# Kernel optimization log

Measured on AMD Instinct MI355X. Metric: run time of the kernel, lower is better.

The kernel has to match this reference:

```python
import jax, jax.numpy as jnp
import numpy as np

NEG_SLOPE = 0.2


def gat_conv(x, src, dst, W, a_src, a_dst, bias, concat, num_nodes):
    # x: [N, F_in]; W: [F_in, H*C]; a_src/a_dst: [H, C]
    H, C = a_src.shape
    h = (x @ W).reshape(num_nodes, H, C)               # [N,H,C]
    alpha_s = jnp.sum(h * a_src[None], axis=-1)        # [N,H]
    alpha_d = jnp.sum(h * a_dst[None], axis=-1)        # [N,H]
    e = jax.nn.leaky_relu(alpha_s[src] + alpha_d[dst], NEG_SLOPE)  # [E,H]
    m = jax.ops.segment_max(e, dst, num_segments=num_nodes)
    m = jnp.where(jnp.isfinite(m), m, 0.0)
    ex = jnp.exp(e - m[dst])
    denom = jax.ops.segment_sum(ex, dst, num_segments=num_nodes)
    alpha = ex / (denom[dst] + 1e-16)                  # scatter-softmax over dst
    msg = h[src] * alpha[:, :, None]                   # [E,H,C]
    out = jax.ops.segment_sum(msg, dst, num_segments=num_nodes)  # [N,H,C]
    if concat:
        out = out.reshape(num_nodes, H * C)
    else:
        out = out.mean(axis=1)
    return out + bias


def setup_inputs() -> dict:
    key = jax.random.key(0)
    ks = jax.random.split(key, 12)
    N, E = 50000, 800000
    num_concat, F_in, hid, H1, H2, n_cls = 2, 128, 64, 4, 1, 16
    x_list = jax.random.normal(ks[0], (num_concat, N, F_in), dtype=jnp.float32)
    edge_index = jax.random.randint(ks[1], (2, E), 0, N, dtype=jnp.int64)
    s = 0.1
    W1 = jax.random.normal(ks[2], (num_concat, F_in, H1 * hid), dtype=jnp.float32) * s
    att_src1 = jax.random.normal(ks[3], (num_concat, H1, hid), dtype=jnp.float32) * s
    att_dst1 = jax.random.normal(ks[4], (num_concat, H1, hid), dtype=jnp.float32) * s
    bias1 = jnp.zeros((num_concat, H1 * hid), dtype=jnp.float32)
    W2 = jax.random.normal(ks[5], (hid * H1 * num_concat, H2 * n_cls), dtype=jnp.float32) * s
    att_src2 = jax.random.normal(ks[6], (H2, n_cls), dtype=jnp.float32) * s
    att_dst2 = jax.random.normal(ks[7], (H2, n_cls), dtype=jnp.float32) * s
    bias2 = jnp.zeros((n_cls,), dtype=jnp.float32)
    return {"x_list": x_list, "edge_index": edge_index,
            "W1": W1, "att_src1": att_src1, "att_dst1": att_dst1, "bias1": bias1,
            "W2": W2, "att_src2": att_src2, "att_dst2": att_dst2, "bias2": bias2}


def reference(x_list, edge_index, W1, att_src1, att_dst1, bias1, W2, att_src2, att_dst2, bias2):
    num_concat, N, _ = x_list.shape
    loop = jnp.arange(N, dtype=edge_index.dtype)
    src = jnp.concatenate([edge_index[0], loop])  # PyG add_self_loops=True
    dst = jnp.concatenate([edge_index[1], loop])
    hidden = [jax.nn.elu(gat_conv(x_list[k], src, dst, W1[k], att_src1[k], att_dst1[k],
                                  bias1[k], True, N))
              for k in range(num_concat)]
    x = jnp.concatenate(hidden, axis=-1)           # [N, hid*H1*num_concat]
    out = gat_conv(x, src, dst, W2, att_src2, att_dst2, bias2, False, N)
    return out
```

## Files before the change

### kernel.cpp

```cpp
#include <hip/hip_runtime.h>

#define LEAKY(v) ((v) >= 0.0f ? (v) : 0.2f * (v))

typedef __attribute__((ext_vector_type(8))) short bf16x8;
typedef __attribute__((ext_vector_type(4))) float f32x4;

__device__ __forceinline__ unsigned short f2bf(float f) {
    unsigned int u = __float_as_uint(f);
    unsigned int r = u + 0x7FFFu + ((u >> 16) & 1u);
    return (unsigned short)(r >> 16);
}
__device__ __forceinline__ unsigned int pk2(float a, float b) {
    return (unsigned int)f2bf(a) | ((unsigned int)f2bf(b) << 16);
}
__device__ __forceinline__ float lo16(unsigned int u) { return __uint_as_float(u << 16); }
__device__ __forceinline__ float hi16(unsigned int u) { return __uint_as_float(u & 0xFFFF0000u); }


__global__ __launch_bounds__(256) void count_deg(const int* ei, int* deg, int E, int Etot) {
    int i = blockIdx.x * 256 + threadIdx.x;
    if (i >= Etot) return;
    int d = (i < E) ? ei[E + i] : (i - E);
    atomicAdd(&deg[d], 1);
}

__global__ __launch_bounds__(512) void scan_block(const int* deg, int* excl, int* bsum, int n) {
    __shared__ int s[512];
    int t = threadIdx.x;
    int i = blockIdx.x * 512 + t;
    int v = (i < n) ? deg[i] : 0;
    s[t] = v;
    __syncthreads();
    for (int d = 1; d < 512; d <<= 1) {
        int x = 0;
        if (t >= d) x = s[t - d];
        __syncthreads();
        if (t >= d) s[t] += x;
        __syncthreads();
    }
    if (i < n) excl[i] = s[t] - v;
    if (t == 511) bsum[blockIdx.x] = s[511];
}

__global__ __launch_bounds__(512) void scan_sums(const int* bsum, int* boff, int nb) {
    __shared__ int s[512];
    int t = threadIdx.x;
    int v = (t < nb) ? bsum[t] : 0;
    s[t] = v;
    __syncthreads();
    for (int d = 1; d < 512; d <<= 1) {
        int x = 0;
        if (t >= d) x = s[t - d];
        __syncthreads();
        if (t >= d) s[t] += x;
        __syncthreads();
    }
    boff[t] = s[t] - v;
}

__global__ __launch_bounds__(256) void finalize_off(int* csr, int* cursor, const int* boff, int n, int etot) {
    int i = blockIdx.x * 256 + threadIdx.x;
    if (i < n) {
        int v = csr[i] + boff[i >> 9];
        csr[i] = v;
        cursor[i] = v;
    }
    if (i == 0) csr[n] = etot;
}

__global__ __launch_bounds__(256) void scatter_src(const int* ei, int* cursor, int* srcs, int E, int Etot) {
    int i = blockIdx.x * 256 + threadIdx.x;
    if (i >= Etot) return;
    int s, d;
    if (i < E) { s = ei[i]; d = ei[E + i]; }
    else       { s = i - E; d = s; }
    int pos = atomicAdd(&cursor[d], 1);
    srcs[pos] = s;
}


__global__ __launch_bounds__(256) void wpack1(const float* __restrict__ W1, unsigned short* __restrict__ wt1) {
    int id = blockIdx.x * 256 + threadIdx.x;
    if (id >= 8192) return;
    int conv = id >> 12, rem = id & 4095;
    int c = rem >> 4, q = rem & 15;
    const float* src = W1 + (size_t)conv * 32768 + (size_t)(q * 8) * 256 + c;
    float w[8];
#pragma unroll
    for (int j = 0; j < 8; ++j) w[j] = src[j * 256];
    uint4 v;
    v.x = pk2(w[0], w[1]); v.y = pk2(w[2], w[3]);
    v.z = pk2(w[4], w[5]); v.w = pk2(w[6], w[7]);
    *(uint4*)(wt1 + (size_t)conv * 32768 + c * 128 + ((q ^ (c & 7)) << 3)) = v;
}

__global__ __launch_bounds__(256) void wpack2(const float* __restrict__ W2, unsigned short* __restrict__ wt2) {
    int id = blockIdx.x * 256 + threadIdx.x;
    if (id >= 1024) return;
    int s = id >> 6, l = id & 63;
    const float* src = W2 + (size_t)(s * 32 + (l >> 4) * 8) * 16 + (l & 15);
    float w[8];
#pragma unroll
    for (int j = 0; j < 8; ++j) w[j] = src[j * 16];
    uint4 v;
    v.x = pk2(w[0], w[1]); v.y = pk2(w[2], w[3]);
    v.z = pk2(w[4], w[5]); v.w = pk2(w[6], w[7]);
    *(uint4*)(wt2 + (size_t)id * 8) = v;
}


__global__ __launch_bounds__(256) void gemm1_mfma(const float* __restrict__ x_list,
                                                  const unsigned short* __restrict__ wt1,
                                                  const float* __restrict__ asw, const float* __restrict__ adw,
                                                  unsigned short* __restrict__ hp,
                                                  float* __restrict__ aad, int N) {
    __shared__ unsigned short As[64 * 128];
    __shared__ unsigned short Ws[256 * 128];
    int conv = blockIdx.y;
    int t = threadIdx.x;
    int w = t >> 6, l = t & 63;

    const float* xg = x_list + (size_t)conv * N * 128;
#pragma unroll
    for (int p = 0; p < 4; ++p) {
        int id = p * 256 + t;
        int row = id >> 4, q = id & 15;
        int grow = blockIdx.x * 64 + row;
        uint4 v = make_uint4(0, 0, 0, 0);
        if (grow < N) {
            const float* src = xg + (size_t)grow * 128 + q * 8;
            float4 a = *(const float4*)src;
            float4 b = *(const float4*)(src + 4);
            v.x = pk2(a.x, a.y); v.y = pk2(a.z, a.w);
            v.z = pk2(b.x, b.y); v.w = pk2(b.z, b.w);
        }
        *(uint4*)(As + row * 128 + ((q ^ (row & 7)) << 3)) = v;
    }
    const uint4* wsrc = (const uint4*)(wt1 + (size_t)conv * 32768);
#pragma unroll
    for (int p = 0; p < 16; ++p) {
        int id = p * 256 + t;
        *(uint4*)(Ws + (size_t)id * 8) = wsrc[id];
    }
    __syncthreads();

    f32x4 acc[4][4];
#pragma unroll
    for (int mt = 0; mt < 4; ++mt)
#pragma unroll
        for (int nt = 0; nt < 4; ++nt) acc[mt][nt] = (f32x4){0.f, 0.f, 0.f, 0.f};

    int lr = l & 15, lg = l >> 4;
#pragma unroll
    for (int s = 0; s < 4; ++s) {
        int kq = s * 4 + lg;
        bf16x8 af[4], bf[4];
#pragma unroll
        for (int mt = 0; mt < 4; ++mt) {
            int r = mt * 16 + lr;
            af[mt] = *(const bf16x8*)(As + r * 128 + ((kq ^ (r & 7)) << 3));
        }
#pragma unroll
        for (int nt = 0; nt < 4; ++nt) {
            int c = w * 64 + nt * 16 + lr;
            bf[nt] = *(const bf16x8*)(Ws + c * 128 + ((kq ^ (c & 7)) << 3));
        }
#pragma unroll
        for (int mt = 0; mt < 4; ++mt)
#pragma unroll
            for (int nt = 0; nt < 4; ++nt)
                acc[mt][nt] = __builtin_amdgcn_mfma_f32_16x16x32_bf16(bf[nt], af[mt], acc[mt][nt], 0, 0, 0);
    }

    float4 aswv[4], adwv[4];
#pragma unroll
    for (int nt = 0; nt < 4; ++nt) {
        aswv[nt] = *(const float4*)(asw + conv * 256 + w * 64 + nt * 16 + lg * 4);
        adwv[nt] = *(const float4*)(adw + conv * 256 + w * 64 + nt * 16 + lg * 4);
    }
#pragma unroll
    for (int mt = 0; mt < 4; ++mt) {
        int grow = blockIdx.x * 64 + mt * 16 + lr;
        bool ok = grow < N;
        float sv = 0.f, dv = 0.f;
#pragma unroll
        for (int nt = 0; nt < 4; ++nt) {
            f32x4 a = acc[mt][nt];
            if (ok) {
                uint2 pk;
                pk.x = pk2(a[0], a[1]);
                pk.y = pk2(a[2], a[3]);
                *(uint2*)(hp + (size_t)grow * 512 + conv * 256 + w * 64 + nt * 16 + lg * 4) = pk;
            }
            sv += a[0] * aswv[nt].x + a[1] * aswv[nt].y + a[2] * aswv[nt].z + a[3] * aswv[nt].w;
            dv += a[0] * adwv[nt].x + a[1] * adwv[nt].y + a[2] * adwv[nt].z + a[3] * adwv[nt].w;
        }
        sv += __shfl_xor(sv, 16); sv += __shfl_xor(sv, 32);
        dv += __shfl_xor(dv, 16); dv += __shfl_xor(dv, 32);
        if (l < 16 && ok) {
            aad[(size_t)grow * 16 + conv * 4 + w]     = sv;
            aad[(size_t)grow * 16 + 8 + conv * 4 + w] = dv;
        }
    }
}


__global__ __launch_bounds__(256) void agg1_both(const unsigned short* __restrict__ hp,
                                                 const float* __restrict__ aad,
                                                 const int* __restrict__ off, const int* __restrict__ srcs,
                                                 const float* __restrict__ b1,
                                                 unsigned short* __restrict__ x2, int N) {
    int n = blockIdx.x * 4 + (threadIdx.x >> 6);
    int lane = threadIdx.x & 63;
    if (n >= N) return;
    int r0 = off[n], r1 = off[n + 1];
    int ch = lane >> 3;
    float ad_l = aad[(size_t)n * 16 + 8 + ch];

    float acc[8] = {0.f, 0.f, 0.f, 0.f, 0.f, 0.f, 0.f, 0.f};
    float den = 0.f;

    for (int base = r0; base < r1; base += 64) {
        int cnt = min(64, r1 - base);
        int my = (base + lane < r1) ? srcs[base + lane] : 0;
        int j = 0;
        for (; j + 2 <= cnt; j += 2) {
            int s0 = __shfl(my, j);
            int s1 = __shfl(my, j + 1);
            uint4 g0 = *(const uint4*)(hp + (size_t)s0 * 512 + lane * 8);
            uint4 g1 = *(const uint4*)(hp + (size_t)s1 * 512 + lane * 8);
            float a0 = aad[(size_t)s0 * 16 + ch];
            float a1 = aad[(size_t)s1 * 16 + ch];
            float p0 = __expf(LEAKY(a0 + ad_l));
            float p1 = __expf(LEAKY(a1 + ad_l));
            den += p0; den += p1;
            acc[0] += p0 * lo16(g0.x); acc[1] += p0 * hi16(g0.x);
            acc[2] += p0 * lo16(g0.y); acc[3] += p0 * hi16(g0.y);
            acc[4] += p0 * lo16(g0.z); acc[5] += p0 * hi16(g0.z);
            acc[6] += p0 * lo16(g0.w); acc[7] += p0 * hi16(g0.w);
            acc[0] += p1 * lo16(g1.x); acc[1] += p1 * hi16(g1.x);
            acc[2] += p1 * lo16(g1.y); acc[3] += p1 * hi16(g1.y);
            acc[4] += p1 * lo16(g1.z); acc[5] += p1 * hi16(g1.z);
            acc[6] += p1 * lo16(g1.w); acc[7] += p1 * hi16(g1.w);
        }
        if (j < cnt) {
            int s0 = __shfl(my, j);
            uint4 g0 = *(const uint4*)(hp + (size_t)s0 * 512 + lane * 8);
            float a0 = aad[(size_t)s0 * 16 + ch];
            float p0 = __expf(LEAKY(a0 + ad_l));
            den += p0;
            acc[0] += p0 * lo16(g0.x); acc[1] += p0 * hi16(g0.x);
            acc[2] += p0 * lo16(g0.y); acc[3] += p0 * hi16(g0.y);
            acc[4] += p0 * lo16(g0.z); acc[5] += p0 * hi16(g0.z);
            acc[6] += p0 * lo16(g0.w); acc[7] += p0 * hi16(g0.w);
        }
    }

    float inv = 1.f / (den + 1e-16f);
    const float* bp = b1 + lane * 8;
    unsigned int ow[4];
#pragma unroll
    for (int q = 0; q < 4; ++q) {
        float o0 = acc[q * 2 + 0] * inv + bp[q * 2 + 0];
        float o1 = acc[q * 2 + 1] * inv + bp[q * 2 + 1];
        o0 = o0 > 0.f ? o0 : (__expf(o0) - 1.0f);
        o1 = o1 > 0.f ? o1 : (__expf(o1) - 1.0f);
        ow[q] = pk2(o0, o1);
    }
    uint4 ov = make_uint4(ow[0], ow[1], ow[2], ow[3]);
    *(uint4*)(x2 + (size_t)n * 512 + lane * 8) = ov;
}


__global__ __launch_bounds__(256) void gemm2_mfma(const unsigned short* __restrict__ x2,
                                                  const unsigned short* __restrict__ wt2,
                                                  const float* __restrict__ asw2, const float* __restrict__ adw2,
                                                  float* __restrict__ h2,
                                                  float* __restrict__ as2, float* __restrict__ ad2, int N) {
    int t = threadIdx.x;
    int w = t >> 6, l = t & 63;
    int rowbase = (blockIdx.x * 4 + w) * 16;
    if (rowbase >= N) return;
    int lr = l & 15, lg = l >> 4;

    f32x4 acc = (f32x4){0.f, 0.f, 0.f, 0.f};
    const unsigned short* ap = x2 + (size_t)(rowbase + lr) * 512 + lg * 8;
#pragma unroll
    for (int s = 0; s < 16; ++s) {
        bf16x8 av = *(const bf16x8*)(ap + s * 32);
        bf16x8 bv = *(const bf16x8*)(wt2 + ((size_t)s * 64 + l) * 8);
        acc = __builtin_amdgcn_mfma_f32_16x16x32_bf16(av, bv, acc, 0, 0, 0);
    }

    float asv = asw2[lr], adv = adw2[lr];
#pragma unroll
    for (int i = 0; i < 4; ++i) {
        int row = rowbase + lg * 4 + i;
        if (row < N) h2[(size_t)row * 16 + lr] = acc[i];
        float sv = acc[i] * asv, dv = acc[i] * adv;
#pragma unroll
        for (int o = 1; o < 16; o <<= 1) {
            sv += __shfl_xor(sv, o);
            dv += __shfl_xor(dv, o);
        }
        if (lr == 0 && row < N) { as2[row] = sv; ad2[row] = dv; }
    }
}


__global__ __launch_bounds__(256) void agg2(const float* __restrict__ h2,
                                            const float* __restrict__ as2, const float* __restrict__ ad2,
                                            const int* __restrict__ off, const int* __restrict__ srcs,
                                            const float* __restrict__ bias2, float* __restrict__ out, int N) {
    int n = blockIdx.x * 4 + (threadIdx.x >> 6);
    int lane = threadIdx.x & 63;
    if (n >= N) return;
    int r0 = off[n], r1 = off[n + 1];
    float adn = ad2[n];
    int cg = lane & 3, eo = lane >> 2;

    float4 acc = make_float4(0.f, 0.f, 0.f, 0.f);
    float den = 0.f;
    for (int base = r0; base + eo < r1; base += 16) {
        int e = base + eo;
        int s = srcs[e];
        float p = __expf(LEAKY(as2[s] + adn));
        float4 hv = *(const float4*)(h2 + (size_t)s * 16 + cg * 4);
        den += p;
        acc.x += p * hv.x; acc.y += p * hv.y;
        acc.z += p * hv.z; acc.w += p * hv.w;
    }
#pragma unroll
    for (int o = 4; o < 64; o <<= 1) {
        acc.x += __shfl_xor(acc.x, o);
        acc.y += __shfl_xor(acc.y, o);
        acc.z += __shfl_xor(acc.z, o);
        acc.w += __shfl_xor(acc.w, o);
        den   += __shfl_xor(den, o);
    }
    if (eo == 0) {
        float inv = 1.f / (den + 1e-16f);
        float4 b = *(const float4*)(bias2 + cg * 4);
        float4 o4;
        o4.x = acc.x * inv + b.x;
        o4.y = acc.y * inv + b.y;
        o4.z = acc.z * inv + b.z;
        o4.w = acc.w * inv + b.w;
        *(float4*)(out + (size_t)n * 16 + cg * 4) = o4;
    }
}


extern "C" void kernel_launch(void* const* d_in, const int* in_sizes, int n_in,
                              void* d_out, int out_size, void* d_ws, size_t ws_size,
                              hipStream_t stream) {
    const float* x_list = (const float*)d_in[0];
    const int*   ei     = (const int*)d_in[1];
    const float* W1     = (const float*)d_in[2];
    const float* as1w   = (const float*)d_in[3];
    const float* ad1w   = (const float*)d_in[4];
    const float* b1     = (const float*)d_in[5];
    const float* W2     = (const float*)d_in[6];
    const float* as2w   = (const float*)d_in[7];
    const float* ad2w   = (const float*)d_in[8];
    const float* b2     = (const float*)d_in[9];
    float* out = (float*)d_out;

    const int N = in_sizes[0] / 256;
    const int E = in_sizes[1] / 2;
    const int Etot = E + N;

    char* ws = (char*)d_ws;
    size_t woff = 0;
    auto alloc = [&](size_t bytes) {
        char* p = ws + woff;
        woff = (woff + bytes + 255) & ~(size_t)255;
        return p;
    };
    int*   csr    = (int*)alloc((size_t)(N + 1) * 4);
    int*   cursor = (int*)alloc((size_t)N * 4);
    int*   srcs   = (int*)alloc((size_t)Etot * 4);
    int*   bsum   = (int*)alloc(512 * 4);
    int*   boff   = (int*)alloc(512 * 4);
    float* aad    = (float*)alloc((size_t)N * 16 * 4);
    float* as2    = (float*)alloc((size_t)N * 4);
    float* ad2    = (float*)alloc((size_t)N * 4);
    unsigned short* wt1 = (unsigned short*)alloc(2 * 32768 * 2);
    unsigned short* wt2 = (unsigned short*)alloc(16 * 64 * 8 * 2);
    unsigned short* hp  = (unsigned short*)alloc((size_t)N * 512 * 2);
    unsigned short* x2  = (unsigned short*)alloc((size_t)N * 512 * 2);
    float* h2     = (float*)alloc((size_t)N * 16 * 4);

    hipMemsetAsync(cursor, 0, (size_t)N * 4, stream);
    int gE = (Etot + 255) / 256;
    count_deg<<<gE, 256, 0, stream>>>(ei, cursor, E, Etot);
    int nb = (N + 511) / 512;
    scan_block<<<nb, 512, 0, stream>>>(cursor, csr, bsum, N);
    scan_sums<<<1, 512, 0, stream>>>(bsum, boff, nb);
    finalize_off<<<(N + 255) / 256, 256, 0, stream>>>(csr, cursor, boff, N, Etot);
    scatter_src<<<gE, 256, 0, stream>>>(ei, cursor, srcs, E, Etot);

    wpack1<<<32, 256, 0, stream>>>(W1, wt1);
    wpack2<<<4, 256, 0, stream>>>(W2, wt2);

    gemm1_mfma<<<dim3((N + 63) / 64, 2), 256, 0, stream>>>(x_list, wt1, as1w, ad1w, hp, aad, N);
    agg1_both<<<(N + 3) / 4, 256, 0, stream>>>(hp, aad, csr, srcs, b1, x2, N);

    gemm2_mfma<<<(N + 63) / 64, 256, 0, stream>>>(x2, wt2, as2w, ad2w, h2, as2, ad2, N);
    agg2<<<(N + 3) / 4, 256, 0, stream>>>(h2, as2, ad2, csr, srcs, b2, out, N);
}
```

Before: 311.9 us.

## Precompute per-edge attention weights in a separate edge kernel for layer-1 aggregation

Adds a dsts array during CSR construction and a new edge_w1 kernel that computes the exp(leaky(as+ad)) weights for all 8 heads of each edge once and stores them in a per-edge buffer. agg1_both then reads these weights instead of gathering aad per lane and evaluating exp inside the aggregation loop. The two weight-pack kernels are also merged into one launch. This adds an extra pass that writes and rereads about 27 MB of edge weights plus a dsts array, in exchange for removing redundant exp work and scattered aad gathers from the aggregation kernel.

```diff
diff --git a/kernel.cpp b/kernel.cpp
--- a/kernel.cpp
+++ b/kernel.cpp
@@ -68,7 +68,8 @@
     if (i == 0) csr[n] = etot;
 }
 
-__global__ __launch_bounds__(256) void scatter_src(const int* ei, int* cursor, int* srcs, int E, int Etot) {
+__global__ __launch_bounds__(256) void scatter_edge(const int* ei, int* cursor, int* srcs, int* dsts,
+                                                    int E, int Etot) {
     int i = blockIdx.x * 256 + threadIdx.x;
     if (i >= Etot) return;
     int s, d;
@@ -76,36 +77,36 @@
     else       { s = i - E; d = s; }
     int pos = atomicAdd(&cursor[d], 1);
     srcs[pos] = s;
-}
-
-
-__global__ __launch_bounds__(256) void wpack1(const float* __restrict__ W1, unsigned short* __restrict__ wt1) {
+    dsts[pos] = d;
+}
+
+
+__global__ __launch_bounds__(256) void wpack(const float* __restrict__ W1, unsigned short* __restrict__ wt1,
+                                             const float* __restrict__ W2, unsigned short* __restrict__ wt2) {
     int id = blockIdx.x * 256 + threadIdx.x;
-    if (id >= 8192) return;
-    int conv = id >> 12, rem = id & 4095;
-    int c = rem >> 4, q = rem & 15;
-    const float* src = W1 + (size_t)conv * 32768 + (size_t)(q * 8) * 256 + c;
-    float w[8];
-#pragma unroll
-    for (int j = 0; j < 8; ++j) w[j] = src[j * 256];
-    uint4 v;
-    v.x = pk2(w[0], w[1]); v.y = pk2(w[2], w[3]);
-    v.z = pk2(w[4], w[5]); v.w = pk2(w[6], w[7]);
-    *(uint4*)(wt1 + (size_t)conv * 32768 + c * 128 + ((q ^ (c & 7)) << 3)) = v;
-}
-
-__global__ __launch_bounds__(256) void wpack2(const float* __restrict__ W2, unsigned short* __restrict__ wt2) {
-    int id = blockIdx.x * 256 + threadIdx.x;
-    if (id >= 1024) return;
-    int s = id >> 6, l = id & 63;
-    const float* src = W2 + (size_t)(s * 32 + (l >> 4) * 8) * 16 + (l & 15);
-    float w[8];
-#pragma unroll
-    for (int j = 0; j < 8; ++j) w[j] = src[j * 16];
-    uint4 v;
-    v.x = pk2(w[0], w[1]); v.y = pk2(w[2], w[3]);
-    v.z = pk2(w[4], w[5]); v.w = pk2(w[6], w[7]);
-    *(uint4*)(wt2 + (size_t)id * 8) = v;
+    if (id < 8192) {
+        int conv = id >> 12, rem = id & 4095;
+        int c = rem >> 4, q = rem & 15;
+        const float* src = W1 + (size_t)conv * 32768 + (size_t)(q * 8) * 256 + c;
+        float w[8];
+#pragma unroll
+        for (int j = 0; j < 8; ++j) w[j] = src[j * 256];
+        uint4 v;
+        v.x = pk2(w[0], w[1]); v.y = pk2(w[2], w[3]);
+        v.z = pk2(w[4], w[5]); v.w = pk2(w[6], w[7]);
+        *(uint4*)(wt1 + (size_t)conv * 32768 + c * 128 + ((q ^ (c & 7)) << 3)) = v;
+    } else if (id < 9216) {
+        int id2 = id - 8192;
+        int s = id2 >> 6, l = id2 & 63;
+        const float* src = W2 + (size_t)(s * 32 + (l >> 4) * 8) * 16 + (l & 15);
+        float w[8];
+#pragma unroll
+        for (int j = 0; j < 8; ++j) w[j] = src[j * 16];
+        uint4 v;
+        v.x = pk2(w[0], w[1]); v.y = pk2(w[2], w[3]);
+        v.z = pk2(w[4], w[5]); v.w = pk2(w[6], w[7]);
+        *(uint4*)(wt2 + (size_t)id2 * 8) = v;
+    }
 }
 
 
@@ -205,8 +206,32 @@
 }
 
 
+__global__ __launch_bounds__(256) void edge_w1(const int* __restrict__ srcs, const int* __restrict__ dsts,
+                                               const float* __restrict__ aad,
+                                               float* __restrict__ pw, int Etot) {
+    int e = blockIdx.x * 256 + threadIdx.x;
+    if (e >= Etot) return;
+    int s = srcs[e], d = dsts[e];
+    float4 as_lo = *(const float4*)(aad + (size_t)s * 16);
+    float4 as_hi = *(const float4*)(aad + (size_t)s * 16 + 4);
+    float4 ad_lo = *(const float4*)(aad + (size_t)d * 16 + 8);
+    float4 ad_hi = *(const float4*)(aad + (size_t)d * 16 + 12);
+    float4 p0, p1;
+    p0.x = __expf(LEAKY(as_lo.x + ad_lo.x));
+    p0.y = __expf(LEAKY(as_lo.y + ad_lo.y));
+    p0.z = __expf(LEAKY(as_lo.z + ad_lo.z));
+    p0.w = __expf(LEAKY(as_lo.w + ad_lo.w));
+    p1.x = __expf(LEAKY(as_hi.x + ad_hi.x));
+    p1.y = __expf(LEAKY(as_hi.y + ad_hi.y));
+    p1.z = __expf(LEAKY(as_hi.z + ad_hi.z));
+    p1.w = __expf(LEAKY(as_hi.w + ad_hi.w));
+    *(float4*)(pw + (size_t)e * 8)     = p0;
+    *(float4*)(pw + (size_t)e * 8 + 4) = p1;
+}
+
+
 __global__ __launch_bounds__(256) void agg1_both(const unsigned short* __restrict__ hp,
-                                                 const float* __restrict__ aad,
+                                                 const float* __restrict__ pw,
                                                  const int* __restrict__ off, const int* __restrict__ srcs,
                                                  const float* __restrict__ b1,
                                                  unsigned short* __restrict__ x2, int N) {
@@ -215,7 +240,6 @@
     if (n >= N) return;
     int r0 = off[n], r1 = off[n + 1];
     int ch = lane >> 3;
-    float ad_l = aad[(size_t)n * 16 + 8 + ch];
 
     float acc[8] = {0.f, 0.f, 0.f, 0.f, 0.f, 0.f, 0.f, 0.f};
     float den = 0.f;
@@ -229,10 +253,8 @@
             int s1 = __shfl(my, j + 1);
             uint4 g0 = *(const uint4*)(hp + (size_t)s0 * 512 + lane * 8);
             uint4 g1 = *(const uint4*)(hp + (size_t)s1 * 512 + lane * 8);
-            float a0 = aad[(size_t)s0 * 16 + ch];
-            float a1 = aad[(size_t)s1 * 16 + ch];
-            float p0 = __expf(LEAKY(a0 + ad_l));
-            float p1 = __expf(LEAKY(a1 + ad_l));
+            float p0 = pw[(size_t)(base + j) * 8 + ch];
+            float p1 = pw[(size_t)(base + j + 1) * 8 + ch];
             den += p0; den += p1;
             acc[0] += p0 * lo16(g0.x); acc[1] += p0 * hi16(g0.x);
             acc[2] += p0 * lo16(g0.y); acc[3] += p0 * hi16(g0.y);
@@ -246,8 +268,7 @@
         if (j < cnt) {
             int s0 = __shfl(my, j);
             uint4 g0 = *(const uint4*)(hp + (size_t)s0 * 512 + lane * 8);
-            float a0 = aad[(size_t)s0 * 16 + ch];
-            float p0 = __expf(LEAKY(a0 + ad_l));
+            float p0 = pw[(size_t)(base + j) * 8 + ch];
             den += p0;
             acc[0] += p0 * lo16(g0.x); acc[1] += p0 * hi16(g0.x);
             acc[2] += p0 * lo16(g0.y); acc[3] += p0 * hi16(g0.y);
@@ -380,6 +401,7 @@
     int*   csr    = (int*)alloc((size_t)(N + 1) * 4);
     int*   cursor = (int*)alloc((size_t)N * 4);
     int*   srcs   = (int*)alloc((size_t)Etot * 4);
+    int*   dsts   = (int*)alloc((size_t)Etot * 4);
     int*   bsum   = (int*)alloc(512 * 4);
     int*   boff   = (int*)alloc(512 * 4);
     float* aad    = (float*)alloc((size_t)N * 16 * 4);
@@ -390,6 +412,7 @@
     unsigned short* hp  = (unsigned short*)alloc((size_t)N * 512 * 2);
     unsigned short* x2  = (unsigned short*)alloc((size_t)N * 512 * 2);
     float* h2     = (float*)alloc((size_t)N * 16 * 4);
+    float* pw     = (float*)alloc((size_t)Etot * 8 * 4);
 
     hipMemsetAsync(cursor, 0, (size_t)N * 4, stream);
     int gE = (Etot + 255) / 256;
@@ -398,13 +421,13 @@
     scan_block<<<nb, 512, 0, stream>>>(cursor, csr, bsum, N);
     scan_sums<<<1, 512, 0, stream>>>(bsum, boff, nb);
     finalize_off<<<(N + 255) / 256, 256, 0, stream>>>(csr, cursor, boff, N, Etot);
-    scatter_src<<<gE, 256, 0, stream>>>(ei, cursor, srcs, E, Etot);
-
-    wpack1<<<32, 256, 0, stream>>>(W1, wt1);
-    wpack2<<<4, 256, 0, stream>>>(W2, wt2);
+    scatter_edge<<<gE, 256, 0, stream>>>(ei, cursor, srcs, dsts, E, Etot);
+
+    wpack<<<36, 256, 0, stream>>>(W1, wt1, W2, wt2);
 
     gemm1_mfma<<<dim3((N + 63) / 64, 2), 256, 0, stream>>>(x_list, wt1, as1w, ad1w, hp, aad, N);
-    agg1_both<<<(N + 3) / 4, 256, 0, stream>>>(hp, aad, csr, srcs, b1, x2, N);
+    edge_w1<<<gE, 256, 0, stream>>>(srcs, dsts, aad, pw, Etot);
+    agg1_both<<<(N + 3) / 4, 256, 0, stream>>>(hp, pw, csr, srcs, b1, x2, N);
 
     gemm2_mfma<<<(N + 63) / 64, 256, 0, stream>>>(x2, wt2, as2w, ad2w, h2, as2, ad2, N);
     agg2<<<(N + 3) / 4, 256, 0, stream>>>(h2, as2, ad2, csr, srcs, b2, out, N);
```

Measured after the change: 308.5 us. No clear change (-1.1%).
